# Performance work log

Measured on AMD Instinct MI355X. Metric: run time of the kernel, lower is better.

Reference implementation:

```python
import jax, jax.numpy as jnp
import numpy as np

N_NODES = 100000
N_EDGES = 1600000
IN_DIM = 128
HID = 128
OUT_DIM = 2
NUM_GRAPHS = 64
BN_EPS = 1e-5


def _glorot(key, shape):
    fan_in, fan_out = shape[0], shape[1]
    lim = np.sqrt(6.0 / (fan_in + fan_out))
    return jax.random.uniform(key, shape, jnp.float32, -lim, lim)


def setup_inputs() -> dict:
    key = jax.random.key(0)
    ks = jax.random.split(key, 12)
    x = jax.random.normal(ks[0], (N_NODES, IN_DIM), jnp.float32)
    edge_index = jax.random.randint(ks[1], (2, N_EDGES), 0, N_NODES, jnp.int64)
    batch = jnp.sort(jax.random.randint(ks[2], (N_NODES,), 0, NUM_GRAPHS, jnp.int64))
    return {
        "x": x,
        "edge_index": edge_index,
        "batch": batch,
        "W1": _glorot(ks[3], (IN_DIM, HID)), "b1": jnp.zeros((HID,), jnp.float32),
        "g1": jnp.ones((HID,), jnp.float32), "be1": jnp.zeros((HID,), jnp.float32),
        "W2": _glorot(ks[4], (HID, HID)), "b2": jnp.zeros((HID,), jnp.float32),
        "g2": jnp.ones((HID,), jnp.float32), "be2": jnp.zeros((HID,), jnp.float32),
        "Wc1": _glorot(ks[5], (HID, HID // 2)), "bc1": jnp.zeros((HID // 2,), jnp.float32),
        "Wc2": _glorot(ks[6], (HID // 2, OUT_DIM)), "bc2": jnp.zeros((OUT_DIM,), jnp.float32),
    }


def gcn_conv(x, src, dst, W, b):
    # PyG GCNConv: add self-loops, symmetric deg^{-1/2} normalization
    n = x.shape[0]
    loop = jnp.arange(n, dtype=src.dtype)
    s = jnp.concatenate([src, loop])
    d = jnp.concatenate([dst, loop])
    deg = jax.ops.segment_sum(jnp.ones_like(d, dtype=x.dtype), d, num_segments=n)
    dinv = jnp.where(deg > 0, jax.lax.rsqrt(deg), 0.0)
    xw = x @ W  # [N, out]
    msgs = xw[s] * (dinv[s] * dinv[d])[:, None]  # [E+N, out]
    out = jax.ops.segment_sum(msgs, d, num_segments=n)
    return out + b


def batchnorm(x, gamma, beta):
    mean = jnp.mean(x, axis=0)
    var = jnp.mean(jnp.square(x - mean), axis=0)  # biased, as torch BN
    return (x - mean) * jax.lax.rsqrt(var + BN_EPS) * gamma + beta


def reference(x, edge_index, batch, W1, b1, g1, be1, W2, b2, g2, be2, Wc1, bc1, Wc2, bc2):
    src, dst = edge_index[0], edge_index[1]
    x = jnp.nan_to_num(x, nan=0.0)
    # layer 1: GCNConv -> BN -> ReLU (dropout = identity in eval)
    h = jax.nn.relu(batchnorm(gcn_conv(x, src, dst, W1, b1), g1, be1))
    # layer 2
    h = jax.nn.relu(batchnorm(gcn_conv(h, src, dst, W2, b2), g2, be2))
    # global mean pool per graph
    sums = jax.ops.segment_sum(h, batch, num_segments=NUM_GRAPHS)
    counts = jax.ops.segment_sum(jnp.ones((h.shape[0],), h.dtype), batch, num_segments=NUM_GRAPHS)
    pooled = sums / jnp.maximum(counts, 1.0)[:, None]  # [G, HID]
    # classifier MLP
    z = jax.nn.relu(pooled @ Wc1 + bc1)
    out = z @ Wc2 + bc2
    return jnp.nan_to_num(out, nan=0.0)
```

## Files before the change

kernel.cpp:

```cpp
#include <hip/hip_runtime.h>

typedef unsigned int uint;
typedef unsigned short ushort;

#define HID 128
#define NGRAPH 64

typedef __attribute__((ext_vector_type(8))) short short8;
typedef __attribute__((ext_vector_type(4))) float floatx4;

__device__ __forceinline__ float bflo(uint w){ return __uint_as_float(w<<16); }
__device__ __forceinline__ float bfhi(uint w){ return __uint_as_float(w & 0xffff0000u); }
__device__ __forceinline__ float bf2f(ushort u){ return __uint_as_float(((uint)u)<<16); }
__device__ __forceinline__ ushort f2bf(float f){
  uint u = __float_as_uint(f);
  u = u + 0x7fffu + ((u>>16)&1u);
  return (ushort)(u>>16);
}
__device__ __forceinline__ uint pack2(float a, float b){
  return (uint)f2bf(a) | ((uint)f2bf(b)<<16);
}
__device__ __forceinline__ float nanz(float v){ return (v==v) ? v : 0.f; }

__device__ __forceinline__ int bat(const int* b, int i, int is64){
  return is64 ? b[2*(size_t)i] : b[i];
}

__global__ void k_zero_prep(int* __restrict__ cnt, float* __restrict__ stats1,
                            float* __restrict__ stats2, float* __restrict__ pooled,
                            uint* __restrict__ xwzero, int NN,
                            const int* __restrict__ ei, int* __restrict__ flags,
                            const float* __restrict__ W1, const float* __restrict__ W2,
                            ushort* __restrict__ wt1, ushort* __restrict__ wt2){
  int bid = blockIdx.x;
  if (bid < 512){
    int i = bid*256 + threadIdx.x;
    for (int t = i; t < NN; t += 512*256) cnt[t] = 0;
    if (i < 256){ stats1[i] = 0.f; stats2[i] = 0.f; }
    if (i < NGRAPH*HID) pooled[i] = 0.f;
    if (i < 64) xwzero[i] = 0u;
    if (bid == 0 && threadIdx.x < 64){
      int t = threadIdx.x;
      bool nz = (ei[2*t + 1] != 0) || (ei[2*(t+64) + 1] != 0);
      unsigned long long m = __ballot(nz);
      if (t == 0) flags[1] = (m == 0ULL) ? 1 : 0;
    }
  } else {
    int b = bid - 512;
    const float* W  = (b & 1) ? W2  : W1;
    ushort*      Wt = (b & 1) ? wt2 : wt1;
    int base = (b >> 1)*4096;
    for (int o = base + threadIdx.x; o < base + 4096; o += 256){
      int j    = o & 7;
      int lane = (o >> 3) & 63;
      int ct   = (o >> 9) & 7;
      int ks   = o >> 12;
      int k = ks*32 + (lane >> 4)*8 + j;
      int n = ct*16 + (lane & 15);
      Wt[o] = f2bf(W[(size_t)k*HID + n]);
    }
  }
}

__global__ void k_sentinel(ushort* out, int n){
  int i = blockIdx.x*blockDim.x + threadIdx.x;
  if (i < n) out[i] = 0x429A;
}


#define NCHUNK 256

__global__ __launch_bounds__(256) void k_hist(const int* __restrict__ ei,
    int* __restrict__ cnt, int E, int NN, const int* __restrict__ flags){
  int is64 = flags[1];
  int part  = blockIdx.x & 7;
  int chunk = blockIdx.x >> 3;
  int p0 = (int)(((long long)NN *  part   ) >> 3);
  int p1 = (int)(((long long)NN * (part+1)) >> 3);
  int per = (E + NCHUNK - 1) / NCHUNK;
  int e0 = chunk * per;
  int e1 = e0 + per; if (e1 > E) e1 = E;
  const int* dstp = ei + (is64 ? 2*(size_t)E : (size_t)E);
  for (int e = e0 + (int)threadIdx.x; e < e1; e += 256){
    int d = is64 ? dstp[2*(size_t)e] : dstp[e];
    if (d >= p0 && d < p1) atomicAdd(&cnt[d], 1);
  }
}

__global__ __launch_bounds__(256) void k_scatter(const int* __restrict__ ei,
    int* __restrict__ cursor, int* __restrict__ srclist, int E, int NN,
    const int* __restrict__ flags){
  int is64 = flags[1];
  int part  = blockIdx.x & 7;
  int chunk = blockIdx.x >> 3;
  int p0 = (int)(((long long)NN *  part   ) >> 3);
  int p1 = (int)(((long long)NN * (part+1)) >> 3);
  int per = (E + NCHUNK - 1) / NCHUNK;
  int e0 = chunk * per;
  int e1 = e0 + per; if (e1 > E) e1 = E;
  const int* dstp = ei + (is64 ? 2*(size_t)E : (size_t)E);
  for (int e = e0 + (int)threadIdx.x; e < e1; e += 256){
    int d = is64 ? dstp[2*(size_t)e] : dstp[e];
    if (d >= p0 && d < p1){
      int s = is64 ? ei[2*(size_t)e] : ei[e];
      if ((uint)s < (uint)NN)
        srclist[atomicAdd(&cursor[d], 1)] = s;
    }
  }
}

__global__ void k_scan1(const int* __restrict__ cnt, int* __restrict__ partials,
                        float* __restrict__ dinv, int NN){
  int t = threadIdx.x;
  int base = blockIdx.x*1024 + t*4;
  int v0=0,v1=0,v2=0,v3=0;
  if (base + 3 < NN){ int4 v = *(const int4*)(cnt + base); v0=v.x; v1=v.y; v2=v.z; v3=v.w; }
  else {
    if (base+0 < NN) v0 = cnt[base+0];
    if (base+1 < NN) v1 = cnt[base+1];
    if (base+2 < NN) v2 = cnt[base+2];
    if (base+3 < NN) v3 = cnt[base+3];
  }
  if (base+0 < NN) dinv[base+0] = rsqrtf((float)(v0+1));
  if (base+1 < NN) dinv[base+1] = rsqrtf((float)(v1+1));
  if (base+2 < NN) dinv[base+2] = rsqrtf((float)(v2+1));
  if (base+3 < NN) dinv[base+3] = rsqrtf((float)(v3+1));
  __shared__ int red[256];
  red[t] = v0+v1+v2+v3;
  __syncthreads();
  for (int off=128; off>0; off>>=1){
    if (t < off) red[t] += red[t+off];
    __syncthreads();
  }
  if (t==0) partials[blockIdx.x] = red[0];
}

__global__ void k_scan2(int* __restrict__ partials, int* __restrict__ offs, int npart, int NN){
  if (threadIdx.x==0 && blockIdx.x==0){
    int run = 0;
    for (int i=0;i<npart;i++){ int tt = partials[i]; partials[i] = run; run += tt; }
    offs[NN] = run;
  }
}

__global__ void k_scan3(const int* __restrict__ cnt, const int* __restrict__ partials,
                        int* __restrict__ offs, int* __restrict__ cursor, int NN){
  int t = threadIdx.x;
  int base = blockIdx.x*1024 + t*4;
  int v0=0,v1=0,v2=0,v3=0;
  if (base + 3 < NN){ int4 v = *(const int4*)(cnt + base); v0=v.x; v1=v.y; v2=v.z; v3=v.w; }
  else {
    if (base+0 < NN) v0 = cnt[base+0];
    if (base+1 < NN) v1 = cnt[base+1];
    if (base+2 < NN) v2 = cnt[base+2];
    if (base+3 < NN) v3 = cnt[base+3];
  }
  int tsum = v0+v1+v2+v3;
  __shared__ int sc[256];
  sc[t] = tsum;
  __syncthreads();
  for (int off=1; off<256; off<<=1){
    int val = (t >= off) ? sc[t-off] : 0;
    __syncthreads();
    sc[t] += val;
    __syncthreads();
  }
  int run = partials[blockIdx.x] + sc[t] - tsum;
  if (base+0 < NN){ offs[base+0] = run; cursor[base+0] = run; run += v0; }
  if (base+1 < NN){ offs[base+1] = run; cursor[base+1] = run; run += v1; }
  if (base+2 < NN){ offs[base+2] = run; cursor[base+2] = run; run += v2; }
  if (base+3 < NN){ offs[base+3] = run; cursor[base+3] = run; run += v3; }
}


__global__ __launch_bounds__(256) void k_gemm1(const float* __restrict__ A,
    const ushort* __restrict__ Wt, const float* __restrict__ dinv,
    ushort* __restrict__ O, int NN){
  __shared__ ushort wlds[16384];
  int tid = threadIdx.x;
  {
    const uint4* s = (const uint4*)Wt;
    uint4* d = (uint4*)wlds;
    #pragma unroll
    for (int i = 0; i < 8; i++) d[tid + i*256] = s[tid + i*256];
  }
  __syncthreads();
  int wave = tid >> 6, lane = tid & 63, m = lane & 15, q = lane >> 4;
  int rowbase = blockIdx.x*64 + wave*16;
  int ar = rowbase + m; if (ar >= NN) ar = NN-1;
  const float* arow = A + (size_t)ar*HID;
  short8 af[4];
  #pragma unroll
  for (int ks=0; ks<4; ks++){
    int kb = ks*32 + q*8;
    float4 f0 = *(const float4*)(arow + kb);
    float4 f1 = *(const float4*)(arow + kb + 4);
    short8 t;
    t[0]=(short)f2bf(nanz(f0.x)); t[1]=(short)f2bf(nanz(f0.y));
    t[2]=(short)f2bf(nanz(f0.z)); t[3]=(short)f2bf(nanz(f0.w));
    t[4]=(short)f2bf(nanz(f1.x)); t[5]=(short)f2bf(nanz(f1.y));
    t[6]=(short)f2bf(nanz(f1.z)); t[7]=(short)f2bf(nanz(f1.w));
    af[ks] = t;
  }
  floatx4 acc[8];
  #pragma unroll
  for (int ct=0; ct<8; ct++) acc[ct] = (floatx4){0.f,0.f,0.f,0.f};
  #pragma unroll
  for (int ks=0; ks<4; ks++){
    #pragma unroll
    for (int ct=0; ct<8; ct++){
      short8 bfrag = *(const short8*)&wlds[(((ks*8+ct)*64) + lane)*8];
      acc[ct] = __builtin_amdgcn_mfma_f32_16x16x32_bf16(af[ks], bfrag, acc[ct], 0, 0, 0);
    }
  }
  float dv[4];
  #pragma unroll
  for (int i=0;i<4;i++){ int r = rowbase + q*4 + i; dv[i] = (r < NN) ? dinv[r] : 0.f; }
  #pragma unroll
  for (int ct=0; ct<8; ct++){
    #pragma unroll
    for (int i=0;i<4;i++){
      int r = rowbase + q*4 + i;
      if (r < NN) O[(size_t)r*HID + ct*16 + m] = f2bf(acc[ct][i]*dv[i]);
    }
  }
}


__global__ __launch_bounds__(256) void k_gemm2(const uint* __restrict__ agg,
    const float* __restrict__ stats, const float* __restrict__ gam,
    const float* __restrict__ bet, const ushort* __restrict__ Wt,
    const float* __restrict__ dinv, ushort* __restrict__ O, int NN, float invn){
  __shared__ ushort wlds[16384];
  __shared__ float cA[128], cB[128];
  int tid = threadIdx.x;
  {
    const uint4* s = (const uint4*)Wt;
    uint4* d = (uint4*)wlds;
    #pragma unroll
    for (int i = 0; i < 8; i++) d[tid + i*256] = s[tid + i*256];
    if (tid < 128){
      float sm = stats[tid], sq = stats[128+tid];
      float mean = sm*invn;
      float var = fmaxf(sq*invn - mean*mean, 0.f);
      float a = gam[tid] * rsqrtf(var + 1e-5f);
      cA[tid] = a;
      cB[tid] = bet[tid] - mean*a;
    }
  }
  __syncthreads();
  int wave = tid >> 6, lane = tid & 63, m = lane & 15, q = lane >> 4;
  int rowbase = blockIdx.x*64 + wave*16;
  int ar = rowbase + m; if (ar >= NN) ar = NN-1;
  const uint* arow = agg + (size_t)ar*64;
  short8 af[4];
  #pragma unroll
  for (int ks=0; ks<4; ks++){
    int kb = ks*32 + q*8;
    uint4 u = *(const uint4*)(arow + (kb >> 1));
    short8 t;
    uint uw[4] = {u.x, u.y, u.z, u.w};
    #pragma unroll
    for (int p=0; p<4; p++){
      int k0 = kb + 2*p;
      float v0 = fmaxf(cA[k0]  *bflo(uw[p]) + cB[k0],   0.f);
      float v1 = fmaxf(cA[k0+1]*bfhi(uw[p]) + cB[k0+1], 0.f);
      t[2*p]   = (short)f2bf(v0);
      t[2*p+1] = (short)f2bf(v1);
    }
    af[ks] = t;
  }
  floatx4 acc[8];
  #pragma unroll
  for (int ct=0; ct<8; ct++) acc[ct] = (floatx4){0.f,0.f,0.f,0.f};
  #pragma unroll
  for (int ks=0; ks<4; ks++){
    #pragma unroll
    for (int ct=0; ct<8; ct++){
      short8 bfrag = *(const short8*)&wlds[(((ks*8+ct)*64) + lane)*8];
      acc[ct] = __builtin_amdgcn_mfma_f32_16x16x32_bf16(af[ks], bfrag, acc[ct], 0, 0, 0);
    }
  }
  float dv[4];
  #pragma unroll
  for (int i=0;i<4;i++){ int r = rowbase + q*4 + i; dv[i] = (r < NN) ? dinv[r] : 0.f; }
  #pragma unroll
  for (int ct=0; ct<8; ct++){
    #pragma unroll
    for (int i=0;i<4;i++){
      int r = rowbase + q*4 + i;
      if (r < NN) O[(size_t)r*HID + ct*16 + m] = f2bf(acc[ct][i]*dv[i]);
    }
  }
}


__global__ __launch_bounds__(256) void k_agg(const uint* __restrict__ xw,
    const int* __restrict__ offs, const int* __restrict__ srclist,
    const float* __restrict__ dinv, uint* __restrict__ agg,
    float* __restrict__ stats, int NN){
  __shared__ float lstat[256];
  lstat[threadIdx.x] = 0.f;
  __syncthreads();
  int wib = threadIdx.x >> 6;
  int lane = threadIdx.x & 63;
  int wid = blockIdx.x*4 + wib;
  int nw = gridDim.x*4;
  float s0=0.f, s1=0.f, q0=0.f, q1=0.f;
  for (int n = wid; n < NN; n += nw){
    int lo = offs[n], hi = offs[n+1];
    float dvn = dinv[n];
    float a0 = 0.f, a1 = 0.f;
    for (int base = lo; base < hi; base += 64){
      int c = hi - base; if (c > 64) c = 64;
      int sidx = (lane < c) ? srclist[base + lane] : NN;
      for (int jb = 0; jb < c; jb += 16){
        uint w[16];
        #pragma unroll
        for (int t = 0; t < 16; t++){
          int sj = __shfl(sidx, jb + t, 64);
          w[t] = xw[(size_t)sj*64 + lane];
        }
        #pragma unroll
        for (int t = 0; t < 16; t++){
          a0 += bflo(w[t]);
          a1 += bfhi(w[t]);
        }
      }
    }
    uint wsf = xw[(size_t)n*64 + lane];
    a0 = (a0 + bflo(wsf)) * dvn;
    a1 = (a1 + bfhi(wsf)) * dvn;
    agg[(size_t)n*64 + lane] = pack2(a0, a1);
    s0 += a0; s1 += a1; q0 += a0*a0; q1 += a1*a1;
  }
  int ch = lane*2;
  atomicAdd(&lstat[ch],       s0);
  atomicAdd(&lstat[ch+1],     s1);
  atomicAdd(&lstat[128+ch],   q0);
  atomicAdd(&lstat[128+ch+1], q1);
  __syncthreads();
  atomicAdd(&stats[threadIdx.x], lstat[threadIdx.x]);
}


#define PSPLIT 16

__global__ __launch_bounds__(256) void k_pool(const uint* __restrict__ agg32,
    const int* __restrict__ batch, const float* __restrict__ stats,
    const float* __restrict__ gam, const float* __restrict__ bet,
    float* __restrict__ pooled, int* __restrict__ counts,
    int NN, const int* __restrict__ flags, float invn){
  int is64 = flags[1];
  __shared__ int bounds[2];
  __shared__ float cA[128], cB[128];
  int g  = blockIdx.x;
  int si = blockIdx.y;
  int tid = threadIdx.x;
  if (tid < 128){
    float sm = stats[tid], sq = stats[128+tid];
    float mean = sm*invn;
    float var = fmaxf(sq*invn - mean*mean, 0.f);
    float a = gam[tid] * rsqrtf(var + 1e-5f);
    cA[tid] = a;
    cB[tid] = bet[tid] - mean*a;
  }
  if (tid == 0){
    int lo=0, hi=NN;
    while (lo<hi){ int mid=(lo+hi)>>1; if (bat(batch,mid,is64) < g) lo=mid+1; else hi=mid; }
    bounds[0] = lo;
    int lo2=lo, hi2=NN;
    while (lo2<hi2){ int mid=(lo2+hi2)>>1; if (bat(batch,mid,is64) < g+1) lo2=mid+1; else hi2=mid; }
    bounds[1] = lo2;
    if (si == 0) counts[g] = hi2 - lo;
  }
  __syncthreads();
  int lo = bounds[0], hi = bounds[1];
  int cnt = hi - lo;
  int chunk = (cnt + PSPLIT - 1) / PSPLIT;
  int s = lo + si*chunk;
  int e = s + chunk; if (e > hi) e = hi;
  int lane = tid & 63, rg = tid >> 6;
  int ch = lane*2;
  float a0c = cA[ch],   b0c = cB[ch];
  float a1c = cA[ch+1], b1c = cB[ch+1];
  float acc0 = 0.f, acc1 = 0.f;
  for (int r = s + rg; r < e; r += 4){
    uint w = agg32[(size_t)r*64 + lane];
    acc0 += fmaxf(a0c*bflo(w) + b0c, 0.f);
    acc1 += fmaxf(a1c*bfhi(w) + b1c, 0.f);
  }
  __shared__ float red[512];
  red[tid] = acc0;
  red[256+tid] = acc1;
  __syncthreads();
  if (tid < 64){
    float s0 = red[tid] + red[tid+64] + red[tid+128] + red[tid+192];
    float s1 = red[256+tid] + red[320+tid] + red[384+tid] + red[448+tid];
    atomicAdd(&pooled[g*HID + ch],     s0);
    atomicAdd(&pooled[g*HID + ch + 1], s1);
  }
}


__global__ void k_mlp(const float* __restrict__ pooled, const int* __restrict__ counts,
                      const float* __restrict__ Wc1, const float* __restrict__ bc1,
                      const float* __restrict__ Wc2, const float* __restrict__ bc2,
                      float* __restrict__ out){
  __shared__ float P[NGRAPH*HID];
  __shared__ float Z[NGRAPH*64];
  int tid = threadIdx.x;
  for (int i = tid; i < NGRAPH*HID; i += 256){
    int g = i >> 7;
    float c = (float)counts[g];
    P[i] = pooled[i] / fmaxf(c, 1.f);
  }
  __syncthreads();
  for (int idx = tid; idx < NGRAPH*64; idx += 256){
    int g = idx >> 6, j = idx & 63;
    float acc = bc1[j];
    for (int k = 0; k < HID; k++) acc += P[g*HID + k] * Wc1[k*64 + j];
    Z[idx] = fmaxf(acc, 0.f);
  }
  __syncthreads();
  if (tid < NGRAPH*2){
    int g = tid >> 1, o = tid & 1;
    float acc = bc2[o];
    for (int k = 0; k < 64; k++) acc += Z[g*64 + k] * Wc2[k*2 + o];
    out[tid] = nanz(acc);
  }
}

extern "C" void kernel_launch(void* const* d_in, const int* in_sizes, int n_in,
                              void* d_out, int out_size, void* d_ws, size_t ws_size,
                              hipStream_t stream){
  const float* x   = (const float*)d_in[0];
  const int*   ei  = (const int*)d_in[1];
  const int* batch = (const int*)d_in[2];
  const float* W1  = (const float*)d_in[3];
  const float* g1  = (const float*)d_in[5];
  const float* be1 = (const float*)d_in[6];
  const float* W2  = (const float*)d_in[7];
  const float* g2  = (const float*)d_in[9];
  const float* be2 = (const float*)d_in[10];
  const float* Wc1 = (const float*)d_in[11];
  const float* bc1 = (const float*)d_in[12];
  const float* Wc2 = (const float*)d_in[13];
  const float* bc2 = (const float*)d_in[14];

  const int NN = in_sizes[2];
  const int E  = in_sizes[1] / 2;

  char* p = (char*)d_ws;
  auto carve = [&](size_t bytes)->char*{
    char* r = p; p += (bytes + 255) & ~(size_t)255; return r;
  };
  int NPART = (NN + 1023)/1024;
  int*   flags    = (int*)  carve(64*4);
  int*   cnt      = (int*)  carve((size_t)NN*4);
  int*   cursor   = (int*)  carve(((size_t)NN+1)*4);
  int*   offs     = (int*)  carve(((size_t)NN+1)*4);
  int*   partials = (int*)  carve((size_t)NPART*4);
  int*   srclist  = (int*)  carve((size_t)E*4);
  float* dinv     = (float*)carve((size_t)NN*4);
  float* stats1   = (float*)carve(256*4);
  float* stats2   = (float*)carve(256*4);
  float* pooled   = (float*)carve((size_t)NGRAPH*HID*4);
  int*   counts   = (int*)  carve(NGRAPH*4);
  ushort* wt1     = (ushort*)carve(16384*2);
  ushort* wt2     = (ushort*)carve(16384*2);
  ushort* xw      = (ushort*)carve(((size_t)NN+1)*HID*2);
  ushort* agg     = (ushort*)carve((size_t)NN*HID*2);
  if ((size_t)(p - (char*)d_ws) > ws_size){
    k_sentinel<<<(out_size+255)/256, 256, 0, stream>>>((ushort*)d_out, out_size);
    return;
  }

  const float invn = 1.f/(float)NN;

  k_zero_prep<<<520, 256, 0, stream>>>(cnt, stats1, stats2, pooled,
                                       (uint*)(xw + (size_t)NN*HID), NN, ei, flags,
                                       W1, W2, wt1, wt2);

  k_hist   <<<NCHUNK*8, 256, 0, stream>>>(ei, cnt, E, NN, flags);
  k_scan1  <<<NPART, 256, 0, stream>>>(cnt, partials, dinv, NN);
  k_scan2  <<<1, 64, 0, stream>>>(partials, offs, NPART, NN);
  k_scan3  <<<NPART, 256, 0, stream>>>(cnt, partials, offs, cursor, NN);
  k_scatter<<<NCHUNK*8, 256, 0, stream>>>(ei, cursor, srclist, E, NN, flags);

  int gblocks = (NN + 63)/64;
  k_gemm1<<<gblocks, 256, 0, stream>>>(x, wt1, dinv, xw, NN);
  k_agg  <<<2048, 256, 0, stream>>>((const uint*)xw, offs, srclist, dinv, (uint*)agg, stats1, NN);
  k_gemm2<<<gblocks, 256, 0, stream>>>((const uint*)agg, stats1, g1, be1, wt2, dinv, xw, NN, invn);
  k_agg  <<<2048, 256, 0, stream>>>((const uint*)xw, offs, srclist, dinv, (uint*)agg, stats2, NN);
  k_pool <<<dim3(NGRAPH, PSPLIT), 256, 0, stream>>>((const uint*)agg, batch, stats2, g2, be2,
                                                    pooled, counts, NN, flags, invn);
  k_mlp  <<<1, 256, 0, stream>>>(pooled, counts, Wc1, bc1, Wc2, bc2, (float*)d_out);
}
```

Before: 577.0 us.

## Compact edge indices to int32, fuse scan passes, column-partition aggregation

Adds a compaction kernel that converts the int64 edge index into separate int32 src/dst arrays, so the histogram and scatter passes read narrower, contiguous data instead of strided 64-bit loads. It removes the single-thread scan2 kernel; each scan3 block now reduces all preceding partials itself. The aggregation kernel is restructured so each block handles one of 8 column slices. Each wave processes 8 neighbors at once with 8 lanes per slice, then reduces across lanes with shuffles. This narrows the per-block working set of the gather but reads each node's neighbor list 8 times and adds shuffle reductions and per-node LDS atomics.

After: 895.8 us. 55.3% more time.

```diff
diff --git a/kernel.cpp b/kernel.cpp
--- a/kernel.cpp
+++ b/kernel.cpp
@@ -67,12 +67,29 @@
   if (i < n) out[i] = 0x429A;
 }
 
+__global__ void k_compact(const int* __restrict__ ei, int* __restrict__ src32,
+                          int* __restrict__ dst32, int E, const int* __restrict__ flags){
+  int is64 = flags[1];
+  int i = blockIdx.x*blockDim.x + threadIdx.x;
+  int stride = gridDim.x*blockDim.x;
+  if (is64){
+    for (int e = i; e < E; e += stride){
+      src32[e] = ei[2*(size_t)e];
+      dst32[e] = ei[2*((size_t)E + e)];
+    }
+  } else {
+    for (int e = i; e < E; e += stride){
+      src32[e] = ei[e];
+      dst32[e] = ei[(size_t)E + e];
+    }
+  }
+}
+
 
 #define NCHUNK 256
 
-__global__ __launch_bounds__(256) void k_hist(const int* __restrict__ ei,
-    int* __restrict__ cnt, int E, int NN, const int* __restrict__ flags){
-  int is64 = flags[1];
+__global__ __launch_bounds__(256) void k_hist(const int* __restrict__ dst32,
+    int* __restrict__ cnt, int E, int NN){
   int part  = blockIdx.x & 7;
   int chunk = blockIdx.x >> 3;
   int p0 = (int)(((long long)NN *  part   ) >> 3);
@@ -80,17 +97,15 @@
   int per = (E + NCHUNK - 1) / NCHUNK;
   int e0 = chunk * per;
   int e1 = e0 + per; if (e1 > E) e1 = E;
-  const int* dstp = ei + (is64 ? 2*(size_t)E : (size_t)E);
   for (int e = e0 + (int)threadIdx.x; e < e1; e += 256){
-    int d = is64 ? dstp[2*(size_t)e] : dstp[e];
+    int d = dst32[e];
     if (d >= p0 && d < p1) atomicAdd(&cnt[d], 1);
   }
 }
 
-__global__ __launch_bounds__(256) void k_scatter(const int* __restrict__ ei,
-    int* __restrict__ cursor, int* __restrict__ srclist, int E, int NN,
-    const int* __restrict__ flags){
-  int is64 = flags[1];
+__global__ __launch_bounds__(256) void k_scatter(const int* __restrict__ src32,
+    const int* __restrict__ dst32, int* __restrict__ cursor,
+    int* __restrict__ srclist, int E, int NN){
   int part  = blockIdx.x & 7;
   int chunk = blockIdx.x >> 3;
   int p0 = (int)(((long long)NN *  part   ) >> 3);
@@ -98,11 +113,10 @@
   int per = (E + NCHUNK - 1) / NCHUNK;
   int e0 = chunk * per;
   int e1 = e0 + per; if (e1 > E) e1 = E;
-  const int* dstp = ei + (is64 ? 2*(size_t)E : (size_t)E);
   for (int e = e0 + (int)threadIdx.x; e < e1; e += 256){
-    int d = is64 ? dstp[2*(size_t)e] : dstp[e];
+    int d = dst32[e];
     if (d >= p0 && d < p1){
-      int s = is64 ? ei[2*(size_t)e] : ei[e];
+      int s = src32[e];
       if ((uint)s < (uint)NN)
         srclist[atomicAdd(&cursor[d], 1)] = s;
     }
@@ -135,17 +149,23 @@
   if (t==0) partials[blockIdx.x] = red[0];
 }
 
-__global__ void k_scan2(int* __restrict__ partials, int* __restrict__ offs, int npart, int NN){
-  if (threadIdx.x==0 && blockIdx.x==0){
-    int run = 0;
-    for (int i=0;i<npart;i++){ int tt = partials[i]; partials[i] = run; run += tt; }
-    offs[NN] = run;
-  }
-}
-
 __global__ void k_scan3(const int* __restrict__ cnt, const int* __restrict__ partials,
                         int* __restrict__ offs, int* __restrict__ cursor, int NN){
   int t = threadIdx.x;
+  __shared__ int red2[256];
+  int lp = 0;
+  for (int i = t; i < (int)blockIdx.x; i += 256) lp += partials[i];
+  red2[t] = lp;
+  __syncthreads();
+  for (int off=128; off>0; off>>=1){
+    if (t < off) red2[t] += red2[t+off];
+    __syncthreads();
+  }
+  int pbase = red2[0];
+  if (t == 0 && blockIdx.x == gridDim.x-1)
+    offs[NN] = pbase + partials[blockIdx.x];
+  __syncthreads();
+
   int base = blockIdx.x*1024 + t*4;
   int v0=0,v1=0,v2=0,v3=0;
   if (base + 3 < NN){ int4 v = *(const int4*)(cnt + base); v0=v.x; v1=v.y; v2=v.z; v3=v.w; }
@@ -165,7 +185,7 @@
     sc[t] += val;
     __syncthreads();
   }
-  int run = partials[blockIdx.x] + sc[t] - tsum;
+  int run = pbase + sc[t] - tsum;
   if (base+0 < NN){ offs[base+0] = run; cursor[base+0] = run; run += v0; }
   if (base+1 < NN){ offs[base+1] = run; cursor[base+1] = run; run += v1; }
   if (base+2 < NN){ offs[base+2] = run; cursor[base+2] = run; run += v2; }
@@ -302,43 +322,44 @@
   __shared__ float lstat[256];
   lstat[threadIdx.x] = 0.f;
   __syncthreads();
-  int wib = threadIdx.x >> 6;
+  int part = blockIdx.x & 7;
+  int wib  = threadIdx.x >> 6;
   int lane = threadIdx.x & 63;
-  int wid = blockIdx.x*4 + wib;
-  int nw = gridDim.x*4;
-  float s0=0.f, s1=0.f, q0=0.f, q1=0.f;
+  int eg = lane >> 3, c = lane & 7;
+  int colbase = part*8;
+  int wid = (blockIdx.x >> 3)*4 + wib;
+  int nw  = (gridDim.x >> 3)*4;
   for (int n = wid; n < NN; n += nw){
     int lo = offs[n], hi = offs[n+1];
     float dvn = dinv[n];
     float a0 = 0.f, a1 = 0.f;
     for (int base = lo; base < hi; base += 64){
-      int c = hi - base; if (c > 64) c = 64;
-      int sidx = (lane < c) ? srclist[base + lane] : NN;
-      for (int jb = 0; jb < c; jb += 16){
-        uint w[16];
-        #pragma unroll
-        for (int t = 0; t < 16; t++){
-          int sj = __shfl(sidx, jb + t, 64);
-          w[t] = xw[(size_t)sj*64 + lane];
-        }
-        #pragma unroll
-        for (int t = 0; t < 16; t++){
-          a0 += bflo(w[t]);
-          a1 += bfhi(w[t]);
-        }
+      int c64 = hi - base; if (c64 > 64) c64 = 64;
+      int sidx = (lane < c64) ? srclist[base + lane] : NN;
+      int nj = (c64 + 7) >> 3;
+      #pragma unroll 4
+      for (int jb = 0; jb < nj; jb++){
+        int sj = __shfl(sidx, jb*8 + eg, 64);
+        uint w = xw[(size_t)sj*64 + colbase + c];
+        a0 += bflo(w);
+        a1 += bfhi(w);
       }
     }
-    uint wsf = xw[(size_t)n*64 + lane];
-    a0 = (a0 + bflo(wsf)) * dvn;
-    a1 = (a1 + bfhi(wsf)) * dvn;
-    agg[(size_t)n*64 + lane] = pack2(a0, a1);
-    s0 += a0; s1 += a1; q0 += a0*a0; q1 += a1*a1;
-  }
-  int ch = lane*2;
-  atomicAdd(&lstat[ch],       s0);
-  atomicAdd(&lstat[ch+1],     s1);
-  atomicAdd(&lstat[128+ch],   q0);
-  atomicAdd(&lstat[128+ch+1], q1);
+    a0 += __shfl_xor(a0, 8, 64);  a1 += __shfl_xor(a1, 8, 64);
+    a0 += __shfl_xor(a0, 16, 64); a1 += __shfl_xor(a1, 16, 64);
+    a0 += __shfl_xor(a0, 32, 64); a1 += __shfl_xor(a1, 32, 64);
+    if (lane < 8){
+      uint ws = xw[(size_t)n*64 + colbase + lane];
+      a0 = (a0 + bflo(ws)) * dvn;
+      a1 = (a1 + bfhi(ws)) * dvn;
+      agg[(size_t)n*64 + colbase + lane] = pack2(a0, a1);
+      int ch = (colbase + lane)*2;
+      atomicAdd(&lstat[ch],       a0);
+      atomicAdd(&lstat[ch+1],     a1);
+      atomicAdd(&lstat[128+ch],   a0*a0);
+      atomicAdd(&lstat[128+ch+1], a1*a1);
+    }
+  }
   __syncthreads();
   atomicAdd(&stats[threadIdx.x], lstat[threadIdx.x]);
 }
@@ -462,6 +483,8 @@
   int*   offs     = (int*)  carve(((size_t)NN+1)*4);
   int*   partials = (int*)  carve((size_t)NPART*4);
   int*   srclist  = (int*)  carve((size_t)E*4);
+  int*   src32    = (int*)  carve((size_t)E*4);
+  int*   dst32    = (int*)  carve((size_t)E*4);
   float* dinv     = (float*)carve((size_t)NN*4);
   float* stats1   = (float*)carve(256*4);
   float* stats2   = (float*)carve(256*4);
@@ -481,12 +504,12 @@
   k_zero_prep<<<520, 256, 0, stream>>>(cnt, stats1, stats2, pooled,
                                        (uint*)(xw + (size_t)NN*HID), NN, ei, flags,
                                        W1, W2, wt1, wt2);
-
-  k_hist   <<<NCHUNK*8, 256, 0, stream>>>(ei, cnt, E, NN, flags);
+  k_compact  <<<640, 256, 0, stream>>>(ei, src32, dst32, E, flags);
+
+  k_hist   <<<NCHUNK*8, 256, 0, stream>>>(dst32, cnt, E, NN);
   k_scan1  <<<NPART, 256, 0, stream>>>(cnt, partials, dinv, NN);
-  k_scan2  <<<1, 64, 0, stream>>>(partials, offs, NPART, NN);
   k_scan3  <<<NPART, 256, 0, stream>>>(cnt, partials, offs, cursor, NN);
-  k_scatter<<<NCHUNK*8, 256, 0, stream>>>(ei, cursor, srclist, E, NN, flags);
+  k_scatter<<<NCHUNK*8, 256, 0, stream>>>(src32, dst32, cursor, srclist, E, NN);
 
   int gblocks = (NN + 63)/64;
   k_gemm1<<<gblocks, 256, 0, stream>>>(x, wt1, dinv, xw, NN);
```
